# Optimization experiments

Hardware: AMD Instinct MI355X
Metric: run time of the kernel (lower is better)

## Reference

```python
import jax, jax.numpy as jnp
import numpy as np

D_MODEL = 2048
NUM_HEADS = 16
D_K = D_MODEL // NUM_HEADS


def setup_inputs() -> dict:
    key = jax.random.key(0)
    ks = jax.random.split(key, 9)
    s = 1.0 / np.sqrt(D_MODEL)
    x = jax.random.normal(ks[0], (4, 4096, D_MODEL), dtype=jnp.float32)
    wq = jax.random.uniform(ks[1], (D_MODEL, D_MODEL), jnp.float32, -s, s)
    bq = jax.random.uniform(ks[2], (D_MODEL,), jnp.float32, -s, s)
    wk = jax.random.uniform(ks[3], (D_MODEL, D_MODEL), jnp.float32, -s, s)
    bk = jax.random.uniform(ks[4], (D_MODEL,), jnp.float32, -s, s)
    wv = jax.random.uniform(ks[5], (D_MODEL, D_MODEL), jnp.float32, -s, s)
    bv = jax.random.uniform(ks[6], (D_MODEL,), jnp.float32, -s, s)
    wo = jax.random.uniform(ks[7], (D_MODEL, D_MODEL), jnp.float32, -s, s)
    bo = jax.random.uniform(ks[8], (D_MODEL,), jnp.float32, -s, s)
    return {"x": x, "wq": wq, "bq": bq, "wk": wk, "bk": bk,
            "wv": wv, "bv": bv, "wo": wo, "bo": bo}


def _heads(t, B, S):
    # (B, S, d_model) -> (B, H, S, d_k)
    return t.reshape(B, S, NUM_HEADS, D_K).transpose(0, 2, 1, 3)


def reference(x, wq, bq, wk, bk, wv, bv, wo, bo):
    B, S, _ = x.shape
    Q = _heads(x @ wq.T + bq, B, S)
    K = _heads(x @ wk.T + bk, B, S)
    V = _heads(x @ wv.T + bv, B, S)
    # elu(x)+1 feature map
    Q = jax.nn.elu(Q) + 1.0
    K = jax.nn.elu(K) + 1.0
    # KV: (B,H,d_k,d_k)
    KV = jnp.einsum('bhsd,bhse->bhde', K, V)
    QKV = jnp.einsum('bhsd,bhde->bhse', Q, KV)
    K_sum = jnp.sum(K, axis=-2)                      # (B,H,d_k)
    QK_sum = jnp.einsum('bhsd,bhd->bhs', Q, K_sum)   # (B,H,S)
    out = QKV / (QK_sum[..., None] + 1e-8)
    out = out.transpose(0, 2, 1, 3).reshape(B, S, D_MODEL)
    return out @ wo.T + bo
```

## Files before the change

### kernel.cpp

```cpp
#include <hip/hip_runtime.h>


#define D_MODEL 2048
#define SEQ     4096
#define BATCH   4
#define HEADS   16
#define DKH     128
#define M_TOK   16384
#define NBH     64

using frag8 = __attribute__((ext_vector_type(8))) short;
using f32x4 = __attribute__((ext_vector_type(4))) float;

typedef __attribute__((address_space(1))) const unsigned int g_u32;
typedef __attribute__((address_space(3))) unsigned int       l_u32;

__device__ __forceinline__ unsigned short f2bf(float f) {
  unsigned u = __float_as_uint(f);
  u = u + 0x7fffu + ((u >> 16) & 1u);
  return (unsigned short)(u >> 16);
}
__device__ __forceinline__ float bf2f(unsigned short h) {
  return __uint_as_float(((unsigned)h) << 16);
}

__global__ __launch_bounds__(256) void convert_f2bf_kernel(
    const float* __restrict__ in, unsigned short* __restrict__ out, int n4) {
  int i = blockIdx.x * 256 + threadIdx.x;
  if (i < n4) {
    float4 v = reinterpret_cast<const float4*>(in)[i];
    ushort4 o;
    o.x = f2bf(v.x); o.y = f2bf(v.y); o.z = f2bf(v.z); o.w = f2bf(v.w);
    reinterpret_cast<ushort4*>(out)[i] = o;
  }
}


__device__ __forceinline__ void stage_tile64(const unsigned short* __restrict__ GA, long lda,
                                             const unsigned short* __restrict__ GB, long ldb,
                                             unsigned short* __restrict__ L,
                                             int wid, int lane) {
  const int rsub = lane >> 3;
  const int ge   = ((lane & 7) ^ rsub) * 8;
#pragma unroll
  for (int r = 0; r < 4; ++r) {
    const int row = r * 64 + wid * 8 + rsub;
    __builtin_amdgcn_global_load_lds((g_u32*)(GA + (long)row * lda + ge),
                                     (l_u32*)(L + r * 4096 + wid * 512), 16, 0, 0);
  }
#pragma unroll
  for (int r = 0; r < 4; ++r) {
    const int row = r * 64 + wid * 8 + rsub;
    __builtin_amdgcn_global_load_lds((g_u32*)(GB + (long)row * ldb + ge),
                                     (l_u32*)(L + 16384 + r * 4096 + wid * 512), 16, 0, 0);
  }
}

#define DS_AV(MS, KK)                                                         \
  _Pragma("unroll") for (int i_ = 0; i_ < 4; ++i_) {                          \
    const int row_ = wm * 128 + (MS) * 64 + i_ * 16 + lr;                     \
    const int cb_ = (((KK) * 2 + lh * 16) ^ ((lr & 7) << 4)) >> 1;            \
    av[i_] = *(const frag8*)(lA + row_ * 64 + cb_);                           \
  }
#define DS_BV(KK)                                                             \
  _Pragma("unroll") for (int n_ = 0; n_ < 4; ++n_) {                          \
    const int row_ = wn * 64 + n_ * 16 + lr;                                  \
    const int cb_ = (((KK) * 2 + lh * 16) ^ ((lr & 7) << 4)) >> 1;            \
    bv[n_] = *(const frag8*)(lB + row_ * 64 + cb_);                           \
  }
#define MFMA16(MS)                                                            \
  __builtin_amdgcn_s_setprio(1);                                              \
  _Pragma("unroll") for (int i_ = 0; i_ < 4; ++i_)                            \
  _Pragma("unroll") for (int n_ = 0; n_ < 4; ++n_)                            \
    acc[(MS) * 4 + i_][n_] = __builtin_amdgcn_mfma_f32_16x16x32_bf16(         \
        av[i_], bv[n_], acc[(MS) * 4 + i_][n_], 0, 0, 0);                     \
  __builtin_amdgcn_s_setprio(0);
#define LGKM0                                                                 \
  asm volatile("s_waitcnt lgkmcnt(0)" ::: "memory");                          \
  __builtin_amdgcn_sched_barrier(0)

template <int MODE, bool XMAJOR>
__global__ __launch_bounds__(512, 2) void gemm256_nt_kernel(
    const unsigned short* __restrict__ A, long lda,
    const unsigned short* __restrict__ Bm, long ldb,
    void* __restrict__ Cv, long ldc,
    const float* __restrict__ bias, int K) {
  __shared__ unsigned short sh[65536];
  const int lane = threadIdx.x & 63, wid = threadIdx.x >> 6;
  const int wm = wid >> 2, wn = wid & 3;
  const int lr = lane & 15, lh = lane >> 4;

  const int gx = gridDim.x, gy = gridDim.y;
  const int cpx = (gx * gy) >> 3;
  const int P = blockIdx.y * gx + blockIdx.x;
  const int L = (P & 7) * cpx + (P >> 3);
  int bx, by;
  if (XMAJOR) { bx = L / gy; by = L - bx * gy; }
  else        { by = L / gx; bx = L - by * gx; }

  const long m0 = (long)by * 256, n0 = (long)bx * 256;
  const unsigned short* Ablk = A + m0 * lda;
  const unsigned short* Bblk = Bm + n0 * ldb;
  const int NT = K >> 6;

  f32x4 acc[8][4];
#pragma unroll
  for (int m = 0; m < 8; ++m)
#pragma unroll
    for (int n = 0; n < 4; ++n) acc[m][n] = (f32x4){0.f, 0.f, 0.f, 0.f};

  stage_tile64(Ablk, lda, Bblk, ldb, sh, wid, lane);
  if (NT > 1)
    stage_tile64(Ablk + 64, lda, Bblk + 64, ldb, sh + 32768, wid, lane);

  for (int t = 0; t < NT; ++t) {
    const unsigned short* lA = sh + (t & 1) * 32768;
    const unsigned short* lB = lA + 16384;
    if (t >= 1 && t + 1 < NT)
      stage_tile64(Ablk + (long)(t + 1) * 64, lda, Bblk + (long)(t + 1) * 64, ldb,
                   (unsigned short*)sh + ((t + 1) & 1) * 32768, wid, lane);
    if (t + 1 < NT) asm volatile("s_waitcnt vmcnt(8)" ::: "memory");
    else            asm volatile("s_waitcnt vmcnt(0)" ::: "memory");
    __builtin_amdgcn_s_barrier();
    frag8 av[4], bv[4];
    DS_AV(0, 0); DS_BV(0);
    LGKM0; MFMA16(0);
    DS_AV(1, 0);
    __builtin_amdgcn_s_barrier();
    LGKM0; MFMA16(1);
    DS_AV(0, 32); DS_BV(32);
    __builtin_amdgcn_s_barrier();
    LGKM0; MFMA16(0);
    DS_AV(1, 32);
    __builtin_amdgcn_s_barrier();
    LGKM0; MFMA16(1);
    __builtin_amdgcn_s_barrier();
  }

#pragma unroll
  for (int m = 0; m < 8; ++m)
#pragma unroll
    for (int n = 0; n < 4; ++n)
#pragma unroll
      for (int r = 0; r < 4; ++r) {
        long row = m0 + wm * 128 + (m >> 2) * 64 + (m & 3) * 16 + lh * 4 + r;
        long col = n0 + wn * 64 + n * 16 + lr;
        float v = acc[m][n][r];
        if (MODE == 0) {
          v += bias[col]; v = v > 0.f ? v + 1.f : __expf(v);
          ((unsigned short*)Cv)[row * ldc + col] = f2bf(v);
        } else if (MODE == 1) {
          v += bias[row]; v = v > 0.f ? v + 1.f : __expf(v);
          ((unsigned short*)Cv)[row * ldc + col] = f2bf(v);
        } else if (MODE == 2) {
          v += bias[row];
          ((unsigned short*)Cv)[row * ldc + col] = f2bf(v);
        } else {
          v += bias[col];
          ((float*)Cv)[row * ldc + col] = v;
        }
      }
}

__device__ __forceinline__ void stage_tile(const unsigned short* __restrict__ G,
                                           long ld, unsigned short* __restrict__ L) {
  const int w = threadIdx.x >> 6, l = threadIdx.x & 63;
#pragma unroll
  for (int r = 0; r < 4; ++r) {
    const int chunk = w * 4 + r;
    const int row = chunk * 8 + (l >> 3);
    const int col = (l & 7) * 8;
    __builtin_amdgcn_global_load_lds((g_u32*)(G + (long)row * ld + col),
                                     (l_u32*)(L + chunk * 512), 16, 0, 0);
  }
}

__device__ __forceinline__ void gemm_mainloop(const unsigned short* __restrict__ A, long lda,
                                              const unsigned short* __restrict__ B, long ldb,
                                              int K, unsigned short* lA, unsigned short* lB,
                                              f32x4 acc[4][4]) {
  const int lane = threadIdx.x & 63;
  const int wid  = threadIdx.x >> 6;
  const int wr = wid >> 1, wc = wid & 1;
  const int lr = lane & 15, lh = lane >> 4;
  for (int k0 = 0; k0 < K; k0 += 64) {
    stage_tile(A + k0, lda, lA);
    stage_tile(B + k0, ldb, lB);
    __syncthreads();
#pragma unroll
    for (int kk = 0; kk < 64; kk += 32) {
      frag8 av[4], bv[4];
#pragma unroll
      for (int m = 0; m < 4; ++m)
        av[m] = *reinterpret_cast<const frag8*>(lA + (wr * 64 + m * 16 + lr) * 64 + kk + lh * 8);
#pragma unroll
      for (int n = 0; n < 4; ++n)
        bv[n] = *reinterpret_cast<const frag8*>(lB + (wc * 64 + n * 16 + lr) * 64 + kk + lh * 8);
#pragma unroll
      for (int m = 0; m < 4; ++m)
#pragma unroll
        for (int n = 0; n < 4; ++n)
          acc[m][n] = __builtin_amdgcn_mfma_f32_16x16x32_bf16(av[m], bv[n], acc[m][n], 0, 0, 0);
    }
    __syncthreads();
  }
}

#define ACC_INIT(acc)                                   \
  _Pragma("unroll") for (int m_ = 0; m_ < 4; ++m_)      \
  _Pragma("unroll") for (int n_ = 0; n_ < 4; ++n_)      \
      acc[m_][n_] = (f32x4){0.f, 0.f, 0.f, 0.f};

__global__ __launch_bounds__(256) void kvt_partial_kernel(
    const unsigned short* __restrict__ VT, const unsigned short* __restrict__ KT,
    float* __restrict__ part) {
  __shared__ unsigned short lA[128 * 64], lB[128 * 64];
  const int z = blockIdx.x;
  const int bh = z >> 3, c = z & 7;
  const int b = bh >> 4, h = bh & 15;
  const long tOff = (long)b * SEQ + (long)c * 512;
  const unsigned short* A  = VT + (long)(h * DKH) * M_TOK + tOff;
  const unsigned short* Bm = KT + (long)(h * DKH) * M_TOK + tOff;
  f32x4 acc[4][4];
  ACC_INIT(acc);
  gemm_mainloop(A, M_TOK, Bm, M_TOK, 512, lA, lB, acc);
  const int lane = threadIdx.x & 63, wid = threadIdx.x >> 6;
  const int wr = wid >> 1, wc = wid & 1, lr = lane & 15, lh = lane >> 4;
  float* out = part + (long)z * (DKH * DKH);
#pragma unroll
  for (int m = 0; m < 4; ++m)
#pragma unroll
    for (int n = 0; n < 4; ++n)
#pragma unroll
      for (int r = 0; r < 4; ++r) {
        int row = wr * 64 + m * 16 + lh * 4 + r;
        int col = wc * 64 + n * 16 + lr;
        out[row * DKH + col] = acc[m][n][r];
      }
}

__global__ __launch_bounds__(256) void reduce_kvt_kernel(
    const float* __restrict__ part, unsigned short* __restrict__ kvt) {
  int i = blockIdx.x * 256 + threadIdx.x;
  if (i < NBH * DKH * DKH) {
    int bh = i >> 14, j = i & 16383;
    float s = 0.f;
#pragma unroll
    for (int c = 0; c < 8; ++c) s += part[(((long)bh * 8 + c) << 14) + j];
    kvt[i] = f2bf(s);
  }
}

__global__ __launch_bounds__(256) void ksum_kernel(const unsigned short* __restrict__ KT,
                                                   float* __restrict__ ksum) {
  int gr = blockIdx.x * 4 + (threadIdx.x >> 6);
  int lane = threadIdx.x & 63;
  int bh = gr >> 7, d = gr & 127;
  int b = bh >> 4, h = bh & 15;
  const unsigned short* p = KT + (long)(h * DKH + d) * M_TOK + (long)b * SEQ;
  float s = 0.f;
#pragma unroll
  for (int i = 0; i < 8; ++i) {
    uint4 v = *reinterpret_cast<const uint4*>(p + (i * 64 + lane) * 8);
    unsigned w[4] = {v.x, v.y, v.z, v.w};
#pragma unroll
    for (int j = 0; j < 4; ++j) {
      s += bf2f((unsigned short)(w[j] & 0xffff));
      s += bf2f((unsigned short)(w[j] >> 16));
    }
  }
#pragma unroll
  for (int o = 32; o > 0; o >>= 1) s += __shfl_down(s, o);
  if (lane == 0) ksum[gr] = s;
}

__global__ __launch_bounds__(256) void qsum_kernel(const unsigned short* __restrict__ Q,
                                                   const float* __restrict__ ksum,
                                                   float* __restrict__ qsum) {
  int gr = blockIdx.x * 4 + (threadIdx.x >> 6);
  int lane = threadIdx.x & 63;
  int bh = gr >> 12, s = gr & 4095;
  int b = bh >> 4, h = bh & 15;
  const unsigned short* q = Q + ((long)b * SEQ + s) * D_MODEL + h * DKH + lane * 2;
  unsigned u = *reinterpret_cast<const unsigned*>(q);
  const float* ks = ksum + bh * DKH + lane * 2;
  float sum = bf2f((unsigned short)(u & 0xffff)) * ks[0] +
              bf2f((unsigned short)(u >> 16)) * ks[1];
#pragma unroll
  for (int o = 32; o > 0; o >>= 1) sum += __shfl_down(sum, o);
  if (lane == 0) qsum[gr] = sum;
}

__global__ __launch_bounds__(256) void qkv_kernel(const unsigned short* __restrict__ Q,
                                                  const unsigned short* __restrict__ KVT,
                                                  const float* __restrict__ qsum,
                                                  unsigned short* __restrict__ attn) {
  __shared__ unsigned short lA[128 * 64], lB[128 * 64];
  const int z = blockIdx.z, b = z >> 4, h = z & 15;
  const long m0 = (long)blockIdx.y * 128;
  const unsigned short* A  = Q + ((long)b * SEQ + m0) * D_MODEL + h * DKH;
  const unsigned short* Bm = KVT + (long)z * (DKH * DKH);
  f32x4 acc[4][4];
  ACC_INIT(acc);
  gemm_mainloop(A, D_MODEL, Bm, DKH, DKH, lA, lB, acc);
  const int lane = threadIdx.x & 63, wid = threadIdx.x >> 6;
  const int wr = wid >> 1, wc = wid & 1, lr = lane & 15, lh = lane >> 4;
#pragma unroll
  for (int m = 0; m < 4; ++m)
#pragma unroll
    for (int n = 0; n < 4; ++n)
#pragma unroll
      for (int r = 0; r < 4; ++r) {
        long row = m0 + wr * 64 + m * 16 + lh * 4 + r;
        int  col = wc * 64 + n * 16 + lr;
        float dnm = qsum[(long)z * SEQ + row] + 1e-8f;
        float v = acc[m][n][r] / dnm;
        attn[((long)b * SEQ + row) * D_MODEL + h * DKH + col] = f2bf(v);
      }
}

#define OFF_XB   0L
#define OFF_WQ   (OFF_XB + (long)M_TOK * D_MODEL * 2)
#define OFF_WK   (OFF_WQ + (long)D_MODEL * D_MODEL * 2)
#define OFF_WV   (OFF_WK + (long)D_MODEL * D_MODEL * 2)
#define OFF_WO   (OFF_WV + (long)D_MODEL * D_MODEL * 2)
#define OFF_QB   (OFF_WO + (long)D_MODEL * D_MODEL * 2)
#define OFF_KT   (OFF_QB + (long)M_TOK * D_MODEL * 2)
#define OFF_VT   (OFF_KT + (long)M_TOK * D_MODEL * 2)
#define OFF_PART (OFF_VT + (long)M_TOK * D_MODEL * 2)
#define OFF_KVT  (OFF_PART + (long)512 * DKH * DKH * 4)
#define OFF_KSUM (OFF_KVT + (long)NBH * DKH * DKH * 2)
#define OFF_QSUM (OFF_KSUM + (long)NBH * DKH * 4)
#define OFF_ATTN OFF_XB

extern "C" void kernel_launch(void* const* d_in, const int* in_sizes, int n_in,
                              void* d_out, int out_size, void* d_ws, size_t ws_size,
                              hipStream_t stream) {
  const float* x  = (const float*)d_in[0];
  const float* wq = (const float*)d_in[1];
  const float* bq = (const float*)d_in[2];
  const float* wk = (const float*)d_in[3];
  const float* bk = (const float*)d_in[4];
  const float* wv = (const float*)d_in[5];
  const float* bv = (const float*)d_in[6];
  const float* wo = (const float*)d_in[7];
  const float* bo = (const float*)d_in[8];

  char* ws = (char*)d_ws;
  unsigned short* xb   = (unsigned short*)(ws + OFF_XB);
  unsigned short* wqb  = (unsigned short*)(ws + OFF_WQ);
  unsigned short* wkb  = (unsigned short*)(ws + OFF_WK);
  unsigned short* wvb  = (unsigned short*)(ws + OFF_WV);
  unsigned short* wob  = (unsigned short*)(ws + OFF_WO);
  unsigned short* Qb   = (unsigned short*)(ws + OFF_QB);
  unsigned short* KTb  = (unsigned short*)(ws + OFF_KT);
  unsigned short* VTb  = (unsigned short*)(ws + OFF_VT);
  float*          part = (float*)(ws + OFF_PART);
  unsigned short* KVTb = (unsigned short*)(ws + OFF_KVT);
  float*          ksum = (float*)(ws + OFF_KSUM);
  float*          qsum = (float*)(ws + OFF_QSUM);
  unsigned short* attn = (unsigned short*)(ws + OFF_ATTN);

  dim3 blk(256);
  dim3 blk5(512);

  convert_f2bf_kernel<<<(M_TOK * D_MODEL / 4) / 256, blk, 0, stream>>>(x, xb, M_TOK * D_MODEL / 4);
  convert_f2bf_kernel<<<(D_MODEL * D_MODEL / 4) / 256, blk, 0, stream>>>(wq, wqb, D_MODEL * D_MODEL / 4);
  convert_f2bf_kernel<<<(D_MODEL * D_MODEL / 4) / 256, blk, 0, stream>>>(wk, wkb, D_MODEL * D_MODEL / 4);
  convert_f2bf_kernel<<<(D_MODEL * D_MODEL / 4) / 256, blk, 0, stream>>>(wv, wvb, D_MODEL * D_MODEL / 4);
  convert_f2bf_kernel<<<(D_MODEL * D_MODEL / 4) / 256, blk, 0, stream>>>(wo, wob, D_MODEL * D_MODEL / 4);

  gemm256_nt_kernel<0, false><<<dim3(D_MODEL / 256, M_TOK / 256), blk5, 0, stream>>>(
      xb, D_MODEL, wqb, D_MODEL, Qb, D_MODEL, bq, D_MODEL);
  gemm256_nt_kernel<1, true><<<dim3(M_TOK / 256, D_MODEL / 256), blk5, 0, stream>>>(
      wkb, D_MODEL, xb, D_MODEL, KTb, M_TOK, bk, D_MODEL);
  gemm256_nt_kernel<2, true><<<dim3(M_TOK / 256, D_MODEL / 256), blk5, 0, stream>>>(
      wvb, D_MODEL, xb, D_MODEL, VTb, M_TOK, bv, D_MODEL);

  kvt_partial_kernel<<<512, blk, 0, stream>>>(VTb, KTb, part);
  reduce_kvt_kernel<<<(NBH * DKH * DKH) / 256, blk, 0, stream>>>(part, KVTb);

  ksum_kernel<<<(NBH * DKH) / 4, blk, 0, stream>>>(KTb, ksum);
  qsum_kernel<<<(NBH * SEQ) / 4, blk, 0, stream>>>(Qb, ksum, qsum);

  qkv_kernel<<<dim3(1, SEQ / 128, NBH), blk, 0, stream>>>(Qb, KVTb, qsum, attn);

  gemm256_nt_kernel<3, false><<<dim3(D_MODEL / 256, M_TOK / 256), blk5, 0, stream>>>(
      attn, D_MODEL, wob, D_MODEL, d_out, D_MODEL, bo, D_MODEL);
}
```

Baseline: 690.3 us.

## Split GEMM k-tiles into half-groups with finer-grained staging and fewer barriers

Restructures the bf16 GEMM main loop so each 64-wide k-tile is staged as two 32-wide groups in a new shared-memory layout. Loads for tile t+2 are issued right after the barrier that frees each half-buffer. This cuts the per-iteration barriers from five to two and overlaps global-to-LDS copies with MFMA work at a finer granularity. The cost is more intricate vmcnt bookkeeping and a new swizzle layout, both of which must be exactly right for correctness.

```diff
diff --git a/kernel.cpp b/kernel.cpp
--- a/kernel.cpp
+++ b/kernel.cpp
@@ -36,37 +36,34 @@
 }
 
 
-__device__ __forceinline__ void stage_tile64(const unsigned short* __restrict__ GA, long lda,
-                                             const unsigned short* __restrict__ GB, long ldb,
-                                             unsigned short* __restrict__ L,
-                                             int wid, int lane) {
-  const int rsub = lane >> 3;
-  const int ge   = ((lane & 7) ^ rsub) * 8;
-#pragma unroll
-  for (int r = 0; r < 4; ++r) {
-    const int row = r * 64 + wid * 8 + rsub;
-    __builtin_amdgcn_global_load_lds((g_u32*)(GA + (long)row * lda + ge),
-                                     (l_u32*)(L + r * 4096 + wid * 512), 16, 0, 0);
-  }
-#pragma unroll
-  for (int r = 0; r < 4; ++r) {
-    const int row = r * 64 + wid * 8 + rsub;
-    __builtin_amdgcn_global_load_lds((g_u32*)(GB + (long)row * ldb + ge),
-                                     (l_u32*)(L + 16384 + r * 4096 + wid * 512), 16, 0, 0);
-  }
-}
-
-#define DS_AV(MS, KK)                                                         \
+__device__ __forceinline__ void stage_group(const unsigned short* __restrict__ GA, long lda,
+                                            const unsigned short* __restrict__ GB, long ldb,
+                                            int kcol, unsigned short* __restrict__ Ldst,
+                                            int wid, int lane) {
+  const int quad = (lane & 7) ^ (lane >> 3);
+  const int rr   = (quad >> 2) * 128 + wid * 16 + (lane >> 3);
+  const int col  = kcol + (quad & 3) * 8;
+#pragma unroll
+  for (int j = 0; j < 2; ++j)
+    __builtin_amdgcn_global_load_lds((g_u32*)(GA + (long)(rr + j * 8) * lda + col),
+                                     (l_u32*)(Ldst + (wid * 128 + j * 64) * 8), 16, 0, 0);
+#pragma unroll
+  for (int j = 0; j < 2; ++j)
+    __builtin_amdgcn_global_load_lds((g_u32*)(GB + (long)(rr + j * 8) * ldb + col),
+                                     (l_u32*)(Ldst + 8192 + (wid * 128 + j * 64) * 8), 16, 0, 0);
+}
+
+#define DS_AV2(LA, MS)                                                        \
   _Pragma("unroll") for (int i_ = 0; i_ < 4; ++i_) {                          \
-    const int row_ = wm * 128 + (MS) * 64 + i_ * 16 + lr;                     \
-    const int cb_ = (((KK) * 2 + lh * 16) ^ ((lr & 7) << 4)) >> 1;            \
-    av[i_] = *(const frag8*)(lA + row_ * 64 + cb_);                           \
-  }
-#define DS_BV(KK)                                                             \
+    const int p_ = (MS) * 64 + i_ * 16 + lr;                                  \
+    const int q_ = (wm * 4 + lh) ^ (lr & 7);                                  \
+    av[i_] = *(const frag8*)((LA) + p_ * 64 + q_ * 8);                        \
+  }
+#define DS_BV2(LB)                                                            \
   _Pragma("unroll") for (int n_ = 0; n_ < 4; ++n_) {                          \
-    const int row_ = wn * 64 + n_ * 16 + lr;                                  \
-    const int cb_ = (((KK) * 2 + lh * 16) ^ ((lr & 7) << 4)) >> 1;            \
-    bv[n_] = *(const frag8*)(lB + row_ * 64 + cb_);                           \
+    const int p_ = (wn & 1) * 64 + n_ * 16 + lr;                              \
+    const int q_ = ((wn >> 1) * 4 + lh) ^ (lr & 7);                           \
+    bv[n_] = *(const frag8*)((LB) + p_ * 64 + q_ * 8);                        \
   }
 #define MFMA16(MS)                                                            \
   __builtin_amdgcn_s_setprio(1);                                              \
@@ -78,6 +75,9 @@
 #define LGKM0                                                                 \
   asm volatile("s_waitcnt lgkmcnt(0)" ::: "memory");                          \
   __builtin_amdgcn_sched_barrier(0)
+#define BARRIER                                                               \
+  __builtin_amdgcn_s_barrier();                                               \
+  __builtin_amdgcn_sched_barrier(0)
 
 template <int MODE, bool XMAJOR>
 __global__ __launch_bounds__(512, 2) void gemm256_nt_kernel(
@@ -93,10 +93,10 @@
   const int gx = gridDim.x, gy = gridDim.y;
   const int cpx = (gx * gy) >> 3;
   const int P = blockIdx.y * gx + blockIdx.x;
-  const int L = (P & 7) * cpx + (P >> 3);
+  const int Lw = (P & 7) * cpx + (P >> 3);
   int bx, by;
-  if (XMAJOR) { bx = L / gy; by = L - bx * gy; }
-  else        { by = L / gx; bx = L - by * gx; }
+  if (XMAJOR) { bx = Lw / gy; by = Lw - bx * gy; }
+  else        { by = Lw / gx; bx = Lw - by * gx; }
 
   const long m0 = (long)by * 256, n0 = (long)bx * 256;
   const unsigned short* Ablk = A + m0 * lda;
@@ -109,32 +109,46 @@
 #pragma unroll
     for (int n = 0; n < 4; ++n) acc[m][n] = (f32x4){0.f, 0.f, 0.f, 0.f};
 
-  stage_tile64(Ablk, lda, Bblk, ldb, sh, wid, lane);
-  if (NT > 1)
-    stage_tile64(Ablk + 64, lda, Bblk + 64, ldb, sh + 32768, wid, lane);
+  stage_group(Ablk, lda, Bblk, ldb, 0,  (unsigned short*)sh,         wid, lane);
+  stage_group(Ablk, lda, Bblk, ldb, 32, (unsigned short*)sh + 16384, wid, lane);
+  if (NT > 1) {
+    stage_group(Ablk, lda, Bblk, ldb, 64, (unsigned short*)sh + 32768, wid, lane);
+    stage_group(Ablk, lda, Bblk, ldb, 96, (unsigned short*)sh + 49152, wid, lane);
+  }
+  asm volatile("s_waitcnt vmcnt(12)" ::: "memory");
+  BARRIER;
 
   for (int t = 0; t < NT; ++t) {
-    const unsigned short* lA = sh + (t & 1) * 32768;
-    const unsigned short* lB = lA + 16384;
-    if (t >= 1 && t + 1 < NT)
-      stage_tile64(Ablk + (long)(t + 1) * 64, lda, Bblk + (long)(t + 1) * 64, ldb,
-                   (unsigned short*)sh + ((t + 1) & 1) * 32768, wid, lane);
-    if (t + 1 < NT) asm volatile("s_waitcnt vmcnt(8)" ::: "memory");
+    const int sl0 = (t & 1) * 2;
+    const unsigned short* lA0 = sh + sl0 * 16384;
+    const unsigned short* lB0 = lA0 + 8192;
+    const unsigned short* lA1 = lA0 + 16384;
+    const unsigned short* lB1 = lA1 + 8192;
+    frag8 av[4], bv[4];
+    DS_AV2(lA0, 0); DS_BV2(lB0);
+    LGKM0; MFMA16(0);
+    DS_AV2(lA0, 1);
+    LGKM0;
+    if (t < NT - 1) asm volatile("s_waitcnt vmcnt(8)" ::: "memory");
     else            asm volatile("s_waitcnt vmcnt(0)" ::: "memory");
-    __builtin_amdgcn_s_barrier();
-    frag8 av[4], bv[4];
-    DS_AV(0, 0); DS_BV(0);
+    BARRIER;
+    if (t + 2 < NT)
+      stage_group(Ablk, lda, Bblk, ldb, (t + 2) * 64,
+                  (unsigned short*)sh + sl0 * 16384, wid, lane);
+    MFMA16(1);
+    DS_AV2(lA1, 0); DS_BV2(lB1);
     LGKM0; MFMA16(0);
-    DS_AV(1, 0);
-    __builtin_amdgcn_s_barrier();
-    LGKM0; MFMA16(1);
-    DS_AV(0, 32); DS_BV(32);
-    __builtin_amdgcn_s_barrier();
-    LGKM0; MFMA16(0);
-    DS_AV(1, 32);
-    __builtin_amdgcn_s_barrier();
-    LGKM0; MFMA16(1);
-    __builtin_amdgcn_s_barrier();
+    DS_AV2(lA1, 1);
+    LGKM0;
+    if (t < NT - 1) {
+      if (t < NT - 2) asm volatile("s_waitcnt vmcnt(8)" ::: "memory");
+      else            asm volatile("s_waitcnt vmcnt(4)" ::: "memory");
+      BARRIER;
+      if (t + 2 < NT)
+        stage_group(Ablk, lda, Bblk, ldb, (t + 2) * 64 + 32,
+                    (unsigned short*)sh + (sl0 + 1) * 16384, wid, lane);
+    }
+    MFMA16(1);
   }
 
 #pragma unroll
```

Measured after the change: 701.4 us. No clear change (+1.6%).
